# Kernel optimization log

Measured on AMD Instinct MI355X. Metric: run time of the kernel, lower is better.

The kernel has to match this reference:

```python
import jax, jax.numpy as jnp
import numpy as np

B, N = 1, 1024
C_A, C_Z, H = 768, 128, 16
CH = C_A // H  # 48
INV_SQRT_CH = float(1.0 / np.sqrt(CH))


def _ln(x, w, b):
    # torch.nn.LayerNorm over last dim, eps=1e-5
    m = jnp.mean(x, axis=-1, keepdims=True)
    v = jnp.mean(jnp.square(x - m), axis=-1, keepdims=True)
    return (x - m) * jax.lax.rsqrt(v + 1e-5) * w + b


def setup_inputs() -> dict:
    key = jax.random.key(0)
    ks = jax.random.split(key, 8)
    rn = lambda k, shape, sc: jax.random.normal(k, shape, dtype=jnp.float32) * sc
    return {
        "a": rn(ks[0], (B, N, C_A), 1.0),
        "z": rn(ks[1], (B, N, N, C_Z), 1.0),
        "mask": jnp.ones((B, N), dtype=jnp.float32),
        "ln_a_w": jnp.ones((C_A,), jnp.float32),
        "ln_a_b": jnp.zeros((C_A,), jnp.float32),
        "ln_z_w": jnp.ones((C_Z,), jnp.float32),
        "ln_z_b": jnp.zeros((C_Z,), jnp.float32),
        "Wq": rn(ks[2], (C_A, H * CH), 0.02),
        "bq": jnp.zeros((H * CH,), jnp.float32),
        "Wk": rn(ks[3], (C_A, H * CH), 0.02),
        "Wv": rn(ks[4], (C_A, H * CH), 0.02),
        "Wb": rn(ks[5], (C_Z, H), 0.02),
        "Wg": rn(ks[6], (C_A, H * CH), 0.02),
        "Wo": rn(ks[7], (H * CH, C_A), 0.02),
    }


def reference(a, z, mask, ln_a_w, ln_a_b, ln_z_w, ln_z_b, Wq, bq, Wk, Wv, Wb, Wg, Wo):
    an = _ln(a, ln_a_w, ln_a_b)                                  # [B, N, C_A]
    q = (an @ Wq + bq).reshape(B, N, H, CH)
    k = (an @ Wk).reshape(B, N, H, CH)
    v = (an @ Wv).reshape(B, N, H, CH)
    # pair bias: LayerNorm(z) -> per-head scalar bias [B, N, N, H]
    bpair = _ln(z, ln_z_w, ln_z_b) @ Wb
    mbias = (mask - 1.0)[:, None, None, :] * 1e9                  # [B, 1, 1, N]
    logits = jnp.einsum('bqhc,bkhc->bhqk', q, k) * INV_SQRT_CH
    logits = logits + jnp.transpose(bpair, (0, 3, 1, 2)) + mbias  # [B, H, N, N]
    attn = jax.nn.softmax(logits, axis=-1)
    o = jnp.einsum('bhqk,bkhc->bqhc', attn, v)                    # [B, N, H, CH]
    g = jax.nn.sigmoid(an @ Wg).reshape(B, N, H, CH)
    out = (g * o).reshape(B, N, H * CH) @ Wo                      # [B, N, C_A]
    return out
```

## Files before the change

kernel.cpp:

```cpp
#include <hip/hip_runtime.h>

#define NSEQ 1024
#define CA   768
#define CZ   128
#define NH   16
#define CHD  48
#define HC   768
#define INV_SQRT_CH 0.14433756729740643f

typedef float v4f __attribute__((ext_vector_type(4)));
typedef short v8s __attribute__((ext_vector_type(8)));

__device__ __forceinline__ short f2bf(float f) {
  union { float f; unsigned u; } v; v.f = f;
  unsigned r = v.u + 0x7fffu + ((v.u >> 16) & 1u);
  return (short)(r >> 16);
}
__device__ __forceinline__ float bf2f(short s) {
  union { unsigned u; float f; } v;
  v.u = ((unsigned)(unsigned short)s) << 16;
  return v.f;
}
__device__ __forceinline__ unsigned cvtpk(float lo, float hi) {
  unsigned r;
  asm("v_cvt_pk_bf16_f32 %0, %1, %2" : "=v"(r) : "v"(lo), "v"(hi));
  return r;
}

__global__ __launch_bounds__(256) void k_front(
    const float* __restrict__ lnzw, const float* __restrict__ lnzb,
    const float* __restrict__ Wb, short* __restrict__ wWp, float* __restrict__ S1bW,
    const float* __restrict__ Wq, const float* __restrict__ Wk,
    const float* __restrict__ Wv, const float* __restrict__ Wg,
    const float* __restrict__ Wo, short* __restrict__ WT, short* __restrict__ WoT,
    const float* __restrict__ a, const float* __restrict__ lnaw,
    const float* __restrict__ lnab, short* __restrict__ anb)
{
  __shared__ __align__(16) char fsm[64 * 65 * 4];
  const int bid = blockIdx.x;
  const int t = threadIdx.x;

  if (bid == 0) {
    const int s = t >> 6, l = t & 63;
    const int r16 = l & 15, cg = l >> 4;
    float v[8];
    #pragma unroll
    for (int j = 0; j < 8; ++j) {
      int d = s * 32 + cg * 8 + j;
      v[j] = lnzw[d] * Wb[d * NH + r16];
    }
    uint4 pk;
    pk.x = cvtpk(v[0], v[1]); pk.y = cvtpk(v[2], v[3]);
    pk.z = cvtpk(v[4], v[5]); pk.w = cvtpk(v[6], v[7]);
    *(uint4*)(wWp + (s * 64 + l) * 8) = pk;
    if (t < NH) {
      float s1 = 0.f, bw = 0.f;
      for (int d = 0; d < CZ; ++d) {
        float wb = Wb[d * NH + t];
        s1 += bf2f(f2bf(lnzw[d] * wb));
        bw += lnzb[d] * wb;
      }
      S1bW[t] = s1;
      S1bW[NH + t] = bw;
    }
  } else if (bid <= 720) {
    float (*tile)[65] = (float(*)[65])fsm;
    const int cb = bid - 1;
    const int mat = cb / 144, rem = cb % 144;
    const int tk = rem % 12, tn = rem / 12;
    const int k0 = tk * 64, n0 = tn * 64;
    const float* __restrict__ W =
        (mat == 0) ? Wq : (mat == 1) ? Wk : (mat == 2) ? Wv : (mat == 3) ? Wg : Wo;
    const float s = (mat == 0) ? INV_SQRT_CH : 1.f;
    const int rr = t >> 4, cc = (t & 15) * 4;
    #pragma unroll
    for (int r = 0; r < 4; ++r) {
      v4f v = *(const v4f*)(W + (size_t)(k0 + r * 16 + rr) * HC + n0 + cc);
      tile[r * 16 + rr][cc + 0] = v[0];
      tile[r * 16 + rr][cc + 1] = v[1];
      tile[r * 16 + rr][cc + 2] = v[2];
      tile[r * 16 + rr][cc + 3] = v[3];
    }
    __syncthreads();
    short* dst = (mat < 4) ? (WT + (size_t)mat * HC * CA) : WoT;
    #pragma unroll
    for (int r = 0; r < 4; ++r) {
      const int nr = r * 16 + rr;
      uint2 pk;
      pk.x = cvtpk(tile[cc + 0][nr] * s, tile[cc + 1][nr] * s);
      pk.y = cvtpk(tile[cc + 2][nr] * s, tile[cc + 3][nr] * s);
      *(uint2*)(dst + (size_t)(n0 + nr) * CA + k0 + cc) = pk;
    }
  } else {
    float* red = (float*)fsm;
    const int row = bid - 721;
    const float* ar = a + (size_t)row * CA;
    float x[3];
    float s = 0.f, s2 = 0.f;
    #pragma unroll
    for (int i = 0; i < 3; ++i) {
      x[i] = ar[t + i * 256];
      s += x[i]; s2 += x[i] * x[i];
    }
    #pragma unroll
    for (int off = 1; off < 64; off <<= 1) {
      s += __shfl_xor(s, off);
      s2 += __shfl_xor(s2, off);
    }
    const int wv = t >> 6;
    if ((t & 63) == 0) { red[wv] = s; red[4 + wv] = s2; }
    __syncthreads();
    s = red[0] + red[1] + red[2] + red[3];
    s2 = red[4] + red[5] + red[6] + red[7];
    const float m = s * (1.f / CA);
    const float var = s2 * (1.f / CA) - m * m;
    const float rs = rsqrtf(var + 1e-5f);
    #pragma unroll
    for (int i = 0; i < 3; ++i) {
      int c = t + i * 256;
      anb[(size_t)row * CA + c] = f2bf((x[i] - m) * rs * lnaw[c] + lnab[c]);
    }
  }
}

__global__ __launch_bounds__(256) void k23_fused(
    const short* __restrict__ anb, const short* __restrict__ WT,
    const float* __restrict__ bq, const float* __restrict__ z,
    const short* __restrict__ wWp, const float* __restrict__ S1bW,
    short* __restrict__ qb, short* __restrict__ kb, short* __restrict__ vT,
    float* __restrict__ gbuf, short* __restrict__ bpair)
{
  __shared__ __align__(16) char smem[20480];
  const int tid = threadIdx.x;
  const int w = tid >> 6, l = tid & 63;
  const int r16 = l & 15, cg = l >> 4;

  if (blockIdx.x < 192) {
    const int bid = blockIdx.x;
    const int bm = bid & 7;
    const int bnb = bid >> 3;
    const int m0 = bm * 128, n0 = bnb * 128;
    const int wr = w >> 1, wc = w & 1;

    short* As = (short*)smem;
    short* Bs = (short*)(smem + 10240);

    const int strow = w * 16 + (l >> 2);
    const int scol = (l & 3) * 8;

    v4f acc[4][4];
    #pragma unroll
    for (int i = 0; i < 4; ++i)
      #pragma unroll
      for (int j = 0; j < 4; ++j)
        acc[i][j] = (v4f){0.f, 0.f, 0.f, 0.f};

    for (int k0 = 0; k0 < CA; k0 += 32) {
      v8s av0 = *(const v8s*)(anb + (size_t)(m0 + strow) * CA + k0 + scol);
      v8s av1 = *(const v8s*)(anb + (size_t)(m0 + 64 + strow) * CA + k0 + scol);
      v8s bv0 = *(const v8s*)(WT + (size_t)(n0 + strow) * CA + k0 + scol);
      v8s bv1 = *(const v8s*)(WT + (size_t)(n0 + 64 + strow) * CA + k0 + scol);
      __syncthreads();
      *(v8s*)(As + (size_t)strow * 40 + scol) = av0;
      *(v8s*)(As + (size_t)(64 + strow) * 40 + scol) = av1;
      *(v8s*)(Bs + (size_t)strow * 40 + scol) = bv0;
      *(v8s*)(Bs + (size_t)(64 + strow) * 40 + scol) = bv1;
      __syncthreads();
      v8s a[4], b[4];
      #pragma unroll
      for (int m = 0; m < 4; ++m)
        a[m] = *(const v8s*)(As + (wr * 64 + m * 16 + r16) * 40 + cg * 8);
      #pragma unroll
      for (int n = 0; n < 4; ++n)
        b[n] = *(const v8s*)(Bs + (wc * 64 + n * 16 + r16) * 40 + cg * 8);
      #pragma unroll
      for (int m = 0; m < 4; ++m)
        #pragma unroll
        for (int n = 0; n < 4; ++n)
          acc[m][n] = __builtin_amdgcn_mfma_f32_16x16x32_bf16(a[m], b[n], acc[m][n], 0, 0, 0);
    }

    const int matsel = n0 / HC;
    #pragma unroll
    for (int n = 0; n < 4; ++n) {
      const int nc = (n0 % HC) + wc * 64 + n * 16 + r16;
      const int rbase = m0 + wr * 64 + cg * 4;
      if (matsel == 0) {
        const float bqs = bq[nc] * INV_SQRT_CH;
        #pragma unroll
        for (int m = 0; m < 4; ++m)
          #pragma unroll
          for (int j = 0; j < 4; ++j)
            qb[(size_t)(rbase + m * 16 + j) * HC + nc] = f2bf(acc[m][n][j] + bqs);
      } else if (matsel == 1) {
        #pragma unroll
        for (int m = 0; m < 4; ++m)
          #pragma unroll
          for (int j = 0; j < 4; ++j)
            kb[(size_t)(rbase + m * 16 + j) * HC + nc] = f2bf(acc[m][n][j]);
      } else if (matsel == 2) {
        #pragma unroll
        for (int m = 0; m < 4; ++m) {
          uint2 pk;
          pk.x = cvtpk(acc[m][n][0], acc[m][n][1]);
          pk.y = cvtpk(acc[m][n][2], acc[m][n][3]);
          *(uint2*)(vT + (size_t)nc * NSEQ + rbase + m * 16) = pk;
        }
      } else {
        #pragma unroll
        for (int m = 0; m < 4; ++m)
          #pragma unroll
          for (int j = 0; j < 4; ++j)
            gbuf[(size_t)(rbase + m * 16 + j) * HC + nc] =
                1.f / (1.f + __expf(-acc[m][n][j]));
      }
    }
  } else {
    const int zbid = blockIdx.x - 192;
    const int q = zbid >> 4;
    const int k0 = (zbid & 15) << 6;
    short* blds = (short*)smem;

    v8s bfrag[4];
    #pragma unroll
    for (int s = 0; s < 4; ++s) bfrag[s] = *(const v8s*)(wWp + (s * 64 + l) * 8);
    const float S1 = S1bW[r16];
    const float bW = S1bW[NH + r16];

    const int krow = k0 + w * 16 + r16;
    const float* __restrict__ zr = z + ((size_t)q * NSEQ + krow) * CZ;
    float sum = 0.f, sum2 = 0.f;
    v8s afrag[4];
    #pragma unroll
    for (int s = 0; s < 4; ++s) {
      v4f z0 = *(const v4f*)(zr + s * 32 + cg * 8);
      v4f z1 = *(const v4f*)(zr + s * 32 + cg * 8 + 4);
      #pragma unroll
      for (int j = 0; j < 4; ++j) {
        sum += z0[j] + z1[j];
        sum2 += z0[j] * z0[j] + z1[j] * z1[j];
      }
      union { v8s s8; unsigned u[4]; } fu;
      fu.u[0] = cvtpk(z0[0], z0[1]);
      fu.u[1] = cvtpk(z0[2], z0[3]);
      fu.u[2] = cvtpk(z1[0], z1[1]);
      fu.u[3] = cvtpk(z1[2], z1[3]);
      afrag[s] = fu.s8;
    }
    sum  += __shfl_xor(sum, 16);  sum  += __shfl_xor(sum, 32);
    sum2 += __shfl_xor(sum2, 16); sum2 += __shfl_xor(sum2, 32);
    const float mean = sum * (1.f / CZ);
    const float var = sum2 * (1.f / CZ) - mean * mean;
    const float rs = rsqrtf(var + 1e-5f);

    v4f acc = {0.f, 0.f, 0.f, 0.f};
    #pragma unroll
    for (int s = 0; s < 4; ++s)
      acc = __builtin_amdgcn_mfma_f32_16x16x32_bf16(afrag[s], bfrag[s], acc, 0, 0, 0);

    float bv[4];
    #pragma unroll
    for (int j = 0; j < 4; ++j) {
      int src = cg * 4 + j;
      float mj = __shfl(mean, src);
      float rj = __shfl(rs, src);
      bv[j] = rj * (acc[j] - mj * S1) + bW;
    }
    uint2 bu;
    bu.x = cvtpk(bv[0], bv[1]);
    bu.y = cvtpk(bv[2], bv[3]);
    *(uint2*)&blds[r16 * 72 + w * 16 + cg * 4] = bu;
    __syncthreads();
    const int h = tid >> 4, kk = (tid & 15) << 2;
    uint2 v = *(const uint2*)&blds[h * 72 + kk];
    *(uint2*)(bpair + (size_t)h * NSEQ * NSEQ + (size_t)q * NSEQ + k0 + kk) = v;
  }
}

#define PL_STRIDE 136
__global__ __launch_bounds__(256) void k4_attn(
    const short* __restrict__ qb, const short* __restrict__ kb,
    const short* __restrict__ vT, const short* __restrict__ bpair,
    const float* __restrict__ mask,
    float* __restrict__ po, float* __restrict__ pm, float* __restrict__ plo)
{
  const int h = blockIdx.x & 15;
  const int qt = (blockIdx.x >> 4) & 15;
  const int ks = blockIdx.x >> 8;
  const int tid = threadIdx.x;
  const int w = tid >> 6, l = tid & 63;
  const int r16 = l & 15, cg = l >> 4;
  const int q0 = qt * 64 + w * 16;
  const int kstart = ks * 256;

  __shared__ __align__(16) short plds[4][16 * PL_STRIDE];
  short* pl = &plds[w][0];

  const v8s vzero = {0, 0, 0, 0, 0, 0, 0, 0};
  v8s qf0, qf1;
  {
    const short* qp = qb + (size_t)(q0 + r16) * HC + h * CHD;
    qf0 = *(const v8s*)(qp + cg * 8);
    qf1 = (cg < 2) ? *(const v8s*)(qp + 32 + cg * 8) : vzero;
  }
  v4f of0 = {0, 0, 0, 0}, of1 = {0, 0, 0, 0}, of2 = {0, 0, 0, 0};
  float mrun[4], lrun[4];
  #pragma unroll
  for (int j = 0; j < 4; ++j) { mrun[j] = -1e30f; lrun[j] = 0.f; }

  const size_t bpb = (size_t)h * NSEQ * NSEQ;

  #pragma unroll
  for (int ch = 0; ch < 2; ++ch) {
    const int k0 = kstart + ch * 128;

    v4f cs[8];
    #pragma unroll
    for (int kt = 0; kt < 8; ++kt) {
      const short* kp = kb + (size_t)(k0 + kt * 16 + r16) * HC + h * CHD;
      v8s b0 = *(const v8s*)(kp + cg * 8);
      v8s b1 = (cg < 2) ? *(const v8s*)(kp + 32 + cg * 8) : vzero;
      v4f tacc = {0.f, 0.f, 0.f, 0.f};
      tacc = __builtin_amdgcn_mfma_f32_16x16x32_bf16(qf0, b0, tacc, 0, 0, 0);
      tacc = __builtin_amdgcn_mfma_f32_16x16x32_bf16(qf1, b1, tacc, 0, 0, 0);
      cs[kt] = tacc;
    }
    #pragma unroll
    for (int kt = 0; kt < 8; ++kt) {
      const int kc = k0 + kt * 16 + r16;
      const float mb = (mask[kc] - 1.f) * 1e9f;
      #pragma unroll
      for (int j = 0; j < 4; ++j) {
        const size_t qo = bpb + (size_t)(q0 + cg * 4 + j) * NSEQ;
        cs[kt][j] += bf2f(bpair[qo + kc]) + mb;
      }
    }
    #pragma unroll
    for (int j = 0; j < 4; ++j) {
      float mx = fmaxf(fmaxf(fmaxf(cs[0][j], cs[1][j]), fmaxf(cs[2][j], cs[3][j])),
                       fmaxf(fmaxf(cs[4][j], cs[5][j]), fmaxf(cs[6][j], cs[7][j])));
      mx = fmaxf(mx, __shfl_xor(mx, 1));
      mx = fmaxf(mx, __shfl_xor(mx, 2));
      mx = fmaxf(mx, __shfl_xor(mx, 4));
      mx = fmaxf(mx, __shfl_xor(mx, 8));
      const float mnew = fmaxf(mrun[j], mx);
      const float alpha = __expf(mrun[j] - mnew);
      mrun[j] = mnew;
      float p[8];
      #pragma unroll
      for (int kt = 0; kt < 8; ++kt) p[kt] = __expf(cs[kt][j] - mnew);
      float rsum = ((p[0] + p[1]) + (p[2] + p[3])) + ((p[4] + p[5]) + (p[6] + p[7]));
      rsum += __shfl_xor(rsum, 1);
      rsum += __shfl_xor(rsum, 2);
      rsum += __shfl_xor(rsum, 4);
      rsum += __shfl_xor(rsum, 8);
      lrun[j] = lrun[j] * alpha + rsum;
      of0[j] *= alpha; of1[j] *= alpha; of2[j] *= alpha;
      const int rowb = (cg * 4 + j) * PL_STRIDE;
      #pragma unroll
      for (int t2 = 0; t2 < 4; ++t2) {
        unsigned u = cvtpk(p[2 * t2], p[2 * t2 + 1]);
        pl[rowb + (2 * t2) * 16 + r16] = (short)u;
        pl[rowb + (2 * t2 + 1) * 16 + r16] = (short)(u >> 16);
      }
    }
    asm volatile("s_waitcnt lgkmcnt(0)" ::: "memory");
    __builtin_amdgcn_sched_barrier(0);
    #pragma unroll
    for (int ks4 = 0; ks4 < 4; ++ks4) {
      v8s pa = *(const v8s*)(pl + r16 * PL_STRIDE + ks4 * 32 + cg * 8);
      const short* vp = vT + (size_t)(h * CHD + r16) * NSEQ + k0 + ks4 * 32 + cg * 8;
      v8s bv0 = *(const v8s*)vp;
      v8s bv1 = *(const v8s*)(vp + 16 * NSEQ);
      v8s bv2 = *(const v8s*)(vp + 32 * NSEQ);
      of0 = __builtin_amdgcn_mfma_f32_16x16x32_bf16(pa, bv0, of0, 0, 0, 0);
      of1 = __builtin_amdgcn_mfma_f32_16x16x32_bf16(pa, bv1, of1, 0, 0, 0);
      of2 = __builtin_amdgcn_mfma_f32_16x16x32_bf16(pa, bv2, of2, 0, 0, 0);
    }
  }

  #pragma unroll
  for (int j = 0; j < 4; ++j) {
    const int q = q0 + cg * 4 + j;
    const size_t rb = (((size_t)ks * NSEQ + q) * NH + h) * CHD + r16;
    po[rb]      = of0[j];
    po[rb + 16] = of1[j];
    po[rb + 32] = of2[j];
    if (r16 == 0) {
      pm[((size_t)ks * NSEQ + q) * NH + h] = mrun[j];
      plo[((size_t)ks * NSEQ + q) * NH + h] = lrun[j];
    }
  }
}

__global__ __launch_bounds__(256) void kcomb(
    const float* __restrict__ po, const float* __restrict__ pm,
    const float* __restrict__ plo, const float* __restrict__ gbuf,
    short* __restrict__ gob)
{
  const int q = blockIdx.x;
  const int t = threadIdx.x;
  const int h = t >> 4, s = t & 15;
  float mi[4], li[4];
  #pragma unroll
  for (int i = 0; i < 4; ++i) {
    mi[i] = pm[((size_t)i * NSEQ + q) * NH + h];
    li[i] = plo[((size_t)i * NSEQ + q) * NH + h];
  }
  float mstar = fmaxf(fmaxf(mi[0], mi[1]), fmaxf(mi[2], mi[3]));
  float wgt[4], L = 0.f;
  #pragma unroll
  for (int i = 0; i < 4; ++i) { wgt[i] = __expf(mi[i] - mstar); L += li[i] * wgt[i]; }
  const float inv = 1.f / L;
  #pragma unroll
  for (int dd = 0; dd < 3; ++dd) {
    const int d = s + dd * 16;
    float o = 0.f;
    #pragma unroll
    for (int i = 0; i < 4; ++i)
      o += po[(((size_t)i * NSEQ + q) * NH + h) * CHD + d] * wgt[i];
    const float gv = gbuf[(size_t)q * HC + h * CHD + d];
    gob[(size_t)q * HC + h * CHD + d] = f2bf(o * inv * gv);
  }
}

__global__ __launch_bounds__(256) void k5_out(
    const short* __restrict__ gob, const short* __restrict__ WoT,
    float* __restrict__ out)
{
  __shared__ __align__(16) short As[128 * 40];
  __shared__ __align__(16) short Bs[128 * 40];
  const int tid = threadIdx.x;
  const int w = tid >> 6, l = tid & 63;
  const int r16 = l & 15, cg = l >> 4;
  const int bm = blockIdx.x & 7;
  const int bn = blockIdx.x >> 3;
  const int m0 = bm * 128, n0 = bn * 128;
  const int wr = w >> 1, wc = w & 1;
  const int strow = w * 16 + (l >> 2);
  const int scol = (l & 3) * 8;

  v4f acc[4][4];
  #pragma unroll
  for (int i = 0; i < 4; ++i)
    #pragma unroll
    for (int j = 0; j < 4; ++j)
      acc[i][j] = (v4f){0.f, 0.f, 0.f, 0.f};

  for (int k0 = 0; k0 < CA; k0 += 32) {
    v8s av0 = *(const v8s*)(gob + (size_t)(m0 + strow) * CA + k0 + scol);
    v8s av1 = *(const v8s*)(gob + (size_t)(m0 + 64 + strow) * CA + k0 + scol);
    v8s bv0 = *(const v8s*)(WoT + (size_t)(n0 + strow) * CA + k0 + scol);
    v8s bv1 = *(const v8s*)(WoT + (size_t)(n0 + 64 + strow) * CA + k0 + scol);
    __syncthreads();
    *(v8s*)(As + (size_t)strow * 40 + scol) = av0;
    *(v8s*)(As + (size_t)(64 + strow) * 40 + scol) = av1;
    *(v8s*)(Bs + (size_t)strow * 40 + scol) = bv0;
    *(v8s*)(Bs + (size_t)(64 + strow) * 40 + scol) = bv1;
    __syncthreads();
    v8s a[4], b[4];
    #pragma unroll
    for (int m = 0; m < 4; ++m)
      a[m] = *(const v8s*)(As + (wr * 64 + m * 16 + r16) * 40 + cg * 8);
    #pragma unroll
    for (int n = 0; n < 4; ++n)
      b[n] = *(const v8s*)(Bs + (wc * 64 + n * 16 + r16) * 40 + cg * 8);
    #pragma unroll
    for (int m = 0; m < 4; ++m)
      #pragma unroll
      for (int n = 0; n < 4; ++n)
        acc[m][n] = __builtin_amdgcn_mfma_f32_16x16x32_bf16(a[m], b[n], acc[m][n], 0, 0, 0);
  }

  #pragma unroll
  for (int n = 0; n < 4; ++n) {
    const int nc = n0 + wc * 64 + n * 16 + r16;
    const int rbase = m0 + wr * 64 + cg * 4;
    #pragma unroll
    for (int m = 0; m < 4; ++m)
      #pragma unroll
      for (int j = 0; j < 4; ++j)
        out[(size_t)(rbase + m * 16 + j) * CA + nc] = acc[m][n][j];
  }
}

extern "C" void kernel_launch(void* const* d_in, const int* in_sizes, int n_in,
                              void* d_out, int out_size, void* d_ws, size_t ws_size,
                              hipStream_t stream) {
  const float* a      = (const float*)d_in[0];
  const float* z      = (const float*)d_in[1];
  const float* mask   = (const float*)d_in[2];
  const float* ln_a_w = (const float*)d_in[3];
  const float* ln_a_b = (const float*)d_in[4];
  const float* ln_z_w = (const float*)d_in[5];
  const float* ln_z_b = (const float*)d_in[6];
  const float* Wq     = (const float*)d_in[7];
  const float* bq     = (const float*)d_in[8];
  const float* Wk     = (const float*)d_in[9];
  const float* Wv     = (const float*)d_in[10];
  const float* Wb     = (const float*)d_in[11];
  const float* Wg     = (const float*)d_in[12];
  const float* Wo     = (const float*)d_in[13];
  float* out = (float*)d_out;

  char* ws = (char*)d_ws;
  short* anb   = (short*)(ws);
  short* WT    = (short*)(ws + (2ull << 20));
  short* WoT   = (short*)(ws + (7ull << 20));
  short* qb    = (short*)(ws + (9ull << 20));
  short* kb    = (short*)(ws + (11ull << 20));
  short* vT    = (short*)(ws + (13ull << 20));
  float* gbuf  = (float*)(ws + (15ull << 20));
  short* wWp   = (short*)(ws + (19ull << 20));
  float* S1bW  = (float*)(ws + (19ull << 20) + 4096ull);
  short* gob   = (short*)(ws + (20ull << 20));
  float* po    = (float*)(ws + (22ull << 20));
  float* pm    = (float*)(ws + (36ull << 20));
  float* plo   = (float*)(ws + (37ull << 20));
  short* bpair = (short*)(ws + (38ull << 20));

  k_front<<<1745, 256, 0, stream>>>(ln_z_w, ln_z_b, Wb, wWp, S1bW,
                                    Wq, Wk, Wv, Wg, Wo, WT, WoT,
                                    a, ln_a_w, ln_a_b, anb);
  k23_fused<<<192 + 16384, 256, 0, stream>>>(anb, WT, bq, z, wWp, S1bW,
                                             qb, kb, vT, gbuf, bpair);
  k4_attn<<<1024, 256, 0, stream>>>(qb, kb, vT, bpair, mask, po, pm, plo);
  kcomb<<<1024, 256, 0, stream>>>(po, pm, plo, gbuf, gob);
  k5_out<<<48, 256, 0, stream>>>(gob, WoT, out);
}
```

Before: 201.7 us.

## Stage pair-bias tiles in LDS and shrink output GEMM tiles for more blocks

The attention kernel now loads each wave's 16x128 pair-bias tile from global memory with vectorized coalesced loads into a per-wave LDS buffer, then reads the bias values from LDS. This replaces scattered 2-byte global gathers. The output projection GEMM switches from 128x128 to 64x64 tiles, launching 192 blocks instead of 48 to fill more compute units. The trade-offs are extra LDS per attention block and less data reuse per block in the GEMM.

```diff
diff --git a/kernel.cpp b/kernel.cpp
--- a/kernel.cpp
+++ b/kernel.cpp
@@ -278,6 +278,7 @@
 }
 
 #define PL_STRIDE 136
+#define BL_STRIDE 144
 __global__ __launch_bounds__(256) void k4_attn(
     const short* __restrict__ qb, const short* __restrict__ kb,
     const short* __restrict__ vT, const short* __restrict__ bpair,
@@ -294,7 +295,9 @@
   const int kstart = ks * 256;
 
   __shared__ __align__(16) short plds[4][16 * PL_STRIDE];
+  __shared__ __align__(16) short blds[4][16 * BL_STRIDE];
   short* pl = &plds[w][0];
+  short* bl = &blds[w][0];
 
   const v8s vzero = {0, 0, 0, 0, 0, 0, 0, 0};
   v8s qf0, qf1;
@@ -309,10 +312,25 @@
   for (int j = 0; j < 4; ++j) { mrun[j] = -1e30f; lrun[j] = 0.f; }
 
   const size_t bpb = (size_t)h * NSEQ * NSEQ;
+  const int srow = l >> 2;
+  const int scol = (l & 3) * 32;
 
   #pragma unroll
   for (int ch = 0; ch < 2; ++ch) {
     const int k0 = kstart + ch * 128;
+
+    {
+      const short* bsrc = bpair + bpb + (size_t)(q0 + srow) * NSEQ + k0 + scol;
+      short* bdst = bl + srow * BL_STRIDE + scol;
+      v8s t0 = *(const v8s*)(bsrc);
+      v8s t1 = *(const v8s*)(bsrc + 8);
+      v8s t2 = *(const v8s*)(bsrc + 16);
+      v8s t3 = *(const v8s*)(bsrc + 24);
+      *(v8s*)(bdst)      = t0;
+      *(v8s*)(bdst + 8)  = t1;
+      *(v8s*)(bdst + 16) = t2;
+      *(v8s*)(bdst + 24) = t3;
+    }
 
     v4f cs[8];
     #pragma unroll
@@ -330,10 +348,8 @@
       const int kc = k0 + kt * 16 + r16;
       const float mb = (mask[kc] - 1.f) * 1e9f;
       #pragma unroll
-      for (int j = 0; j < 4; ++j) {
-        const size_t qo = bpb + (size_t)(q0 + cg * 4 + j) * NSEQ;
-        cs[kt][j] += bf2f(bpair[qo + kc]) + mb;
-      }
+      for (int j = 0; j < 4; ++j)
+        cs[kt][j] += bf2f(bl[(cg * 4 + j) * BL_STRIDE + kt * 16 + r16]) + mb;
     }
     #pragma unroll
     for (int j = 0; j < 4; ++j) {
@@ -428,56 +444,52 @@
     const short* __restrict__ gob, const short* __restrict__ WoT,
     float* __restrict__ out)
 {
-  __shared__ __align__(16) short As[128 * 40];
-  __shared__ __align__(16) short Bs[128 * 40];
+  __shared__ __align__(16) short As[64 * 40];
+  __shared__ __align__(16) short Bs[64 * 40];
   const int tid = threadIdx.x;
   const int w = tid >> 6, l = tid & 63;
   const int r16 = l & 15, cg = l >> 4;
-  const int bm = blockIdx.x & 7;
-  const int bn = blockIdx.x >> 3;
-  const int m0 = bm * 128, n0 = bn * 128;
+  const int bm = blockIdx.x & 15;
+  const int bn = blockIdx.x >> 4;
+  const int m0 = bm * 64, n0 = bn * 64;
   const int wr = w >> 1, wc = w & 1;
-  const int strow = w * 16 + (l >> 2);
-  const int scol = (l & 3) * 8;
-
-  v4f acc[4][4];
-  #pragma unroll
-  for (int i = 0; i < 4; ++i)
-    #pragma unroll
-    for (int j = 0; j < 4; ++j)
+  const int strow = tid >> 2;
+  const int scol = (tid & 3) * 8;
+
+  v4f acc[2][2];
+  #pragma unroll
+  for (int i = 0; i < 2; ++i)
+    #pragma unroll
+    for (int j = 0; j < 2; ++j)
       acc[i][j] = (v4f){0.f, 0.f, 0.f, 0.f};
 
   for (int k0 = 0; k0 < CA; k0 += 32) {
-    v8s av0 = *(const v8s*)(gob + (size_t)(m0 + strow) * CA + k0 + scol);
-    v8s av1 = *(const v8s*)(gob + (size_t)(m0 + 64 + strow) * CA + k0 + scol);
-    v8s bv0 = *(const v8s*)(WoT + (size_t)(n0 + strow) * CA + k0 + scol);
-    v8s bv1 = *(const v8s*)(WoT + (size_t)(n0 + 64 + strow) * CA + k0 + scol);
+    v8s av = *(const v8s*)(gob + (size_t)(m0 + strow) * CA + k0 + scol);
+    v8s bv = *(const v8s*)(WoT + (size_t)(n0 + strow) * CA + k0 + scol);
     __syncthreads();
-    *(v8s*)(As + (size_t)strow * 40 + scol) = av0;
-    *(v8s*)(As + (size_t)(64 + strow) * 40 + scol) = av1;
-    *(v8s*)(Bs + (size_t)strow * 40 + scol) = bv0;
-    *(v8s*)(Bs + (size_t)(64 + strow) * 40 + scol) = bv1;
+    *(v8s*)(As + (size_t)strow * 40 + scol) = av;
+    *(v8s*)(Bs + (size_t)strow * 40 + scol) = bv;
     __syncthreads();
-    v8s a[4], b[4];
-    #pragma unroll
-    for (int m = 0; m < 4; ++m)
-      a[m] = *(const v8s*)(As + (wr * 64 + m * 16 + r16) * 40 + cg * 8);
-    #pragma unroll
-    for (int n = 0; n < 4; ++n)
-      b[n] = *(const v8s*)(Bs + (wc * 64 + n * 16 + r16) * 40 + cg * 8);
-    #pragma unroll
-    for (int m = 0; m < 4; ++m)
-      #pragma unroll
-      for (int n = 0; n < 4; ++n)
+    v8s a[2], b[2];
+    #pragma unroll
+    for (int m = 0; m < 2; ++m)
+      a[m] = *(const v8s*)(As + (wr * 32 + m * 16 + r16) * 40 + cg * 8);
+    #pragma unroll
+    for (int n = 0; n < 2; ++n)
+      b[n] = *(const v8s*)(Bs + (wc * 32 + n * 16 + r16) * 40 + cg * 8);
+    #pragma unroll
+    for (int m = 0; m < 2; ++m)
+      #pragma unroll
+      for (int n = 0; n < 2; ++n)
         acc[m][n] = __builtin_amdgcn_mfma_f32_16x16x32_bf16(a[m], b[n], acc[m][n], 0, 0, 0);
   }
 
   #pragma unroll
-  for (int n = 0; n < 4; ++n) {
-    const int nc = n0 + wc * 64 + n * 16 + r16;
-    const int rbase = m0 + wr * 64 + cg * 4;
-    #pragma unroll
-    for (int m = 0; m < 4; ++m)
+  for (int n = 0; n < 2; ++n) {
+    const int nc = n0 + wc * 32 + n * 16 + r16;
+    const int rbase = m0 + wr * 32 + cg * 4;
+    #pragma unroll
+    for (int m = 0; m < 2; ++m)
       #pragma unroll
       for (int j = 0; j < 4; ++j)
         out[(size_t)(rbase + m * 16 + j) * CA + nc] = acc[m][n][j];
@@ -526,5 +538,5 @@
                                              qb, kb, vT, gbuf, bpair);
   k4_attn<<<1024, 256, 0, stream>>>(qb, kb, vT, bpair, mask, po, pm, plo);
   kcomb<<<1024, 256, 0, stream>>>(po, pm, plo, gbuf, gob);
-  k5_out<<<48, 256, 0, stream>>>(gob, WoT, out);
-}
+  k5_out<<<192, 256, 0, stream>>>(gob, WoT, out);
+}
```

Result: faster. 196.2 us (-2.7%).
